# Performance work log

Measured on AMD Instinct MI355X. Metric: run time of the kernel, lower is better.

The kernel has to match this reference:

```python
import jax, jax.numpy as jnp
import numpy as np

B, L, D = 8, 2048, 1024
LN_EPS = 1e-5
WKV_EPS = 1e-8


def _ln(x, g, b):
    m = x.mean(-1, keepdims=True)
    v = x.var(-1, keepdims=True)  # biased var, matches torch LayerNorm
    return (x - m) * jax.lax.rsqrt(v + LN_EPS) * g + b


def _shift(x):
    # ZeroPad2d((0,0,1,-1)): x_prev[:, t] = x[:, t-1], x_prev[:, 0] = 0
    return jnp.pad(x, ((0, 0), (1, 0), (0, 0)))[:, :-1]


def _wkv(k, v, time_decay, time_first):
    # Faithful to the torch loop: t=0 uses exp(u + k0); t>0 decays prior state
    # (including the u-boosted first term) by exp(-exp(time_decay)).
    ew = jnp.exp(-jnp.exp(time_decay))  # [D]
    e0 = jnp.exp(time_first + k[:, 0])  # [B, D]
    a0 = e0 * v[:, 0]
    b0 = e0

    def step(carry, kv):
        a, b = carry
        kt, vt = kv
        ek = jnp.exp(kt)
        a = ew * a + ek * vt
        b = ew * b + ek
        return (a, b), a / (b + WKV_EPS)

    xs = (jnp.swapaxes(k[:, 1:], 0, 1), jnp.swapaxes(v[:, 1:], 0, 1))  # [L-1, B, D]
    _, outs = jax.lax.scan(step, (a0, b0), xs)
    out0 = (a0 / (b0 + WKV_EPS))[:, None]  # [B, 1, D]
    return jnp.concatenate([out0, jnp.swapaxes(outs, 0, 1)], axis=1)  # [B, L, D]


def setup_inputs() -> dict:
    key = jax.random.key(0)
    ks = jax.random.split(key, 10)
    s = 1.0 / np.sqrt(D)

    def w(k, shape, scale):
        return jax.random.normal(k, shape, jnp.float32) * scale

    return {
        "x": jax.random.normal(ks[0], (B, L, D), jnp.float32),
        "ln1_g": jnp.ones((D,), jnp.float32),
        "ln1_b": jnp.zeros((D,), jnp.float32),
        "Wk": w(ks[1], (D, D), s),
        "Wv": w(ks[2], (D, D), s),
        "Wr": w(ks[3], (D, D), s),
        "Wo": w(ks[4], (D, D), s),
        "time_decay": w(ks[5], (D,), 0.1),
        "time_first": w(ks[6], (D,), 0.1),
        "mix_k": jnp.full((D,), 0.5, jnp.float32),
        "mix_v": jnp.full((D,), 0.5, jnp.float32),
        "mix_r": jnp.full((D,), 0.5, jnp.float32),
        "ln2_g": jnp.ones((D,), jnp.float32),
        "ln2_b": jnp.zeros((D,), jnp.float32),
        "Wfk": w(ks[7], (D, 4 * D), s),
        "Wfv": w(ks[8], (4 * D, D), 1.0 / np.sqrt(4 * D)),
        "Wfr": w(ks[9], (D, D), s),
    }


def reference(x, ln1_g, ln1_b, Wk, Wv, Wr, Wo, time_decay, time_first,
              mix_k, mix_v, mix_r, ln2_g, ln2_b, Wfk, Wfv, Wfr):
    # --- time mixing ---
    xn = _ln(x, ln1_g, ln1_b)
    xp = _shift(xn)
    k = (xn * mix_k + xp * (1.0 - mix_k)) @ Wk
    v = (xn * mix_v + xp * (1.0 - mix_v)) @ Wv
    r = jax.nn.sigmoid((xn * mix_r + xp * (1.0 - mix_r)) @ Wr)
    wkv = _wkv(k, v, time_decay, time_first)
    x = x + (r * wkv) @ Wo
    # --- channel mixing ---
    yn = _ln(x, ln2_g, ln2_b)
    yp = _shift(yn)
    kk = jnp.square(jax.nn.relu((0.5 * yn + 0.5 * yp) @ Wfk))
    rr = jax.nn.sigmoid(yn @ Wfr)
    return x + rr * (kk @ Wfv)
```

## Files before the change

### kernel.cpp

```cpp
#include <hip/hip_runtime.h>
#include <hip/hip_bf16.h>
#include <stdint.h>

typedef __hip_bfloat16 bf16_t;
typedef __attribute__((ext_vector_type(8))) short bf16x8;
typedef __attribute__((ext_vector_type(4))) float f32x4;

#define DEV static __device__ __forceinline__

constexpr int kBB = 8, kL = 2048, kD = 1024;
constexpr int kM = kBB * kL;
constexpr int kSeg = 32, kP = 64;

DEV float bf2f(unsigned short u) { return __uint_as_float((unsigned)u << 16); }
DEV unsigned short f2bf(float f) {
  unsigned u = __float_as_uint(f);
  return (unsigned short)((u + 0x7fffu + ((u >> 16) & 1u)) >> 16);
}

DEV void gld16(const void* g, void* l) {
  const __attribute__((address_space(1))) unsigned* gp =
      (const __attribute__((address_space(1))) unsigned*)(uintptr_t)g;
  __attribute__((address_space(3))) unsigned* lp =
      (__attribute__((address_space(3))) unsigned*)(unsigned)(uintptr_t)l;
  __builtin_amdgcn_global_load_lds(gp, lp, 16, 0, 0);
}

__global__ __launch_bounds__(256) void k_transpose_cast(
    const float* __restrict__ W, bf16_t* __restrict__ Wt, int R, int C) {
  __shared__ float tile[32][33];
  const int bx = blockIdx.x * 32;
  const int by = blockIdx.y * 32;
  const int tx = threadIdx.x & 31, ty = threadIdx.x >> 5;
#pragma unroll
  for (int i = 0; i < 32; i += 8)
    tile[ty + i][tx] = W[(size_t)(by + ty + i) * C + (bx + tx)];
  __syncthreads();
#pragma unroll
  for (int i = 0; i < 32; i += 8)
    Wt[(size_t)(bx + ty + i) * R + (by + tx)] = __float2bfloat16(tile[tx][ty + i]);
}

__global__ __launch_bounds__(256) void k_ln1f(
    const float* __restrict__ X, const float* __restrict__ g, const float* __restrict__ be,
    const float* __restrict__ mk, const float* __restrict__ mv, const float* __restrict__ mr,
    bf16_t* __restrict__ ok, bf16_t* __restrict__ ov, bf16_t* __restrict__ orr) {
  const int row = blockIdx.x;
  const int l = row & (kL - 1);
  const int i = threadIdx.x;
  const bool hp = (l != 0);
  float xa[4], pa[4] = {0.f, 0.f, 0.f, 0.f};
  *(float4*)xa = ((const float4*)(X + (size_t)row * kD))[i];
  if (hp) *(float4*)pa = ((const float4*)(X + (size_t)(row - 1) * kD))[i];
  float s0 = xa[0] + xa[1] + xa[2] + xa[3];
  float q0 = xa[0] * xa[0] + xa[1] * xa[1] + xa[2] * xa[2] + xa[3] * xa[3];
  float s1 = pa[0] + pa[1] + pa[2] + pa[3];
  float q1 = pa[0] * pa[0] + pa[1] * pa[1] + pa[2] * pa[2] + pa[3] * pa[3];
#pragma unroll
  for (int off = 32; off > 0; off >>= 1) {
    s0 += __shfl_xor(s0, off); q0 += __shfl_xor(q0, off);
    s1 += __shfl_xor(s1, off); q1 += __shfl_xor(q1, off);
  }
  __shared__ float red[4][4];
  const int wid = i >> 6, lane = i & 63;
  if (lane == 0) { red[wid][0] = s0; red[wid][1] = q0; red[wid][2] = s1; red[wid][3] = q1; }
  __syncthreads();
  s0 = red[0][0] + red[1][0] + red[2][0] + red[3][0];
  q0 = red[0][1] + red[1][1] + red[2][1] + red[3][1];
  s1 = red[0][2] + red[1][2] + red[2][2] + red[3][2];
  q1 = red[0][3] + red[1][3] + red[2][3] + red[3][3];
  const float m0 = s0 * (1.f / kD);
  const float r0 = rsqrtf(fmaxf(q0 * (1.f / kD) - m0 * m0, 0.f) + 1e-5f);
  const float m1 = s1 * (1.f / kD);
  const float r1 = rsqrtf(fmaxf(q1 * (1.f / kD) - m1 * m1, 0.f) + 1e-5f);
  float ga[4], ba[4], ka[4], va[4], ra[4];
  *(float4*)ga = ((const float4*)g)[i];
  *(float4*)ba = ((const float4*)be)[i];
  *(float4*)ka = ((const float4*)mk)[i];
  *(float4*)va = ((const float4*)mv)[i];
  *(float4*)ra = ((const float4*)mr)[i];
  ushort4 uk, uv, ur;
  unsigned short* pk = (unsigned short*)&uk;
  unsigned short* pv = (unsigned short*)&uv;
  unsigned short* pr = (unsigned short*)&ur;
#pragma unroll
  for (int c = 0; c < 4; ++c) {
    float xn = (xa[c] - m0) * r0 * ga[c] + ba[c];
    float xp = hp ? (pa[c] - m1) * r1 * ga[c] + ba[c] : 0.f;
    pk[c] = f2bf(xn * ka[c] + xp * (1.f - ka[c]));
    pv[c] = f2bf(xn * va[c] + xp * (1.f - va[c]));
    pr[c] = f2bf(xn * ra[c] + xp * (1.f - ra[c]));
  }
  ((ushort4*)(ok + (size_t)row * kD))[i] = uk;
  ((ushort4*)(ov + (size_t)row * kD))[i] = uv;
  ((ushort4*)(orr + (size_t)row * kD))[i] = ur;
}

__global__ __launch_bounds__(256) void k_ln2f(
    const float* __restrict__ X, const float* __restrict__ g, const float* __restrict__ be,
    bf16_t* __restrict__ om, bf16_t* __restrict__ on) {
  const int row = blockIdx.x;
  const int l = row & (kL - 1);
  const int i = threadIdx.x;
  const bool hp = (l != 0);
  float xa[4], pa[4] = {0.f, 0.f, 0.f, 0.f};
  *(float4*)xa = ((const float4*)(X + (size_t)row * kD))[i];
  if (hp) *(float4*)pa = ((const float4*)(X + (size_t)(row - 1) * kD))[i];
  float s0 = xa[0] + xa[1] + xa[2] + xa[3];
  float q0 = xa[0] * xa[0] + xa[1] * xa[1] + xa[2] * xa[2] + xa[3] * xa[3];
  float s1 = pa[0] + pa[1] + pa[2] + pa[3];
  float q1 = pa[0] * pa[0] + pa[1] * pa[1] + pa[2] * pa[2] + pa[3] * pa[3];
#pragma unroll
  for (int off = 32; off > 0; off >>= 1) {
    s0 += __shfl_xor(s0, off); q0 += __shfl_xor(q0, off);
    s1 += __shfl_xor(s1, off); q1 += __shfl_xor(q1, off);
  }
  __shared__ float red[4][4];
  const int wid = i >> 6, lane = i & 63;
  if (lane == 0) { red[wid][0] = s0; red[wid][1] = q0; red[wid][2] = s1; red[wid][3] = q1; }
  __syncthreads();
  s0 = red[0][0] + red[1][0] + red[2][0] + red[3][0];
  q0 = red[0][1] + red[1][1] + red[2][1] + red[3][1];
  s1 = red[0][2] + red[1][2] + red[2][2] + red[3][2];
  q1 = red[0][3] + red[1][3] + red[2][3] + red[3][3];
  const float m0 = s0 * (1.f / kD);
  const float r0 = rsqrtf(fmaxf(q0 * (1.f / kD) - m0 * m0, 0.f) + 1e-5f);
  const float m1 = s1 * (1.f / kD);
  const float r1 = rsqrtf(fmaxf(q1 * (1.f / kD) - m1 * m1, 0.f) + 1e-5f);
  float ga[4], ba[4];
  *(float4*)ga = ((const float4*)g)[i];
  *(float4*)ba = ((const float4*)be)[i];
  ushort4 um, un;
  unsigned short* qm = (unsigned short*)&um;
  unsigned short* qn = (unsigned short*)&un;
#pragma unroll
  for (int c = 0; c < 4; ++c) {
    float yn = (xa[c] - m0) * r0 * ga[c] + ba[c];
    float yp = hp ? (pa[c] - m1) * r1 * ga[c] + ba[c] : 0.f;
    qm[c] = f2bf(0.5f * (yn + yp));
    qn[c] = f2bf(yn);
  }
  ((ushort4*)(om + (size_t)row * kD))[i] = um;
  ((ushort4*)(on + (size_t)row * kD))[i] = un;
}

__global__ __launch_bounds__(256) void k_wkv_seg(
    const unsigned short* __restrict__ kq, const unsigned short* __restrict__ vq,
    const float* __restrict__ td, const float* __restrict__ tf,
    float* __restrict__ segA, float* __restrict__ segB) {
  const int d = blockIdx.x * 256 + threadIdx.x;
  const int b = blockIdx.y;
  const int s = blockIdx.z;
  const float ew = __expf(-__expf(td[d]));
  const float uu = (s == 0) ? tf[d] : 0.f;
  const size_t base = ((size_t)b * kL + (size_t)s * kP) * kD + d;
  float a = 0.f, bb = 0.f;
  unsigned short kA[16], vA[16], kB[16], vB[16];
  auto pref = [&](unsigned short* ka, unsigned short* va, int c) {
    const size_t o0 = base + (size_t)c * 16 * kD;
#pragma unroll
    for (int j = 0; j < 16; ++j) {
      ka[j] = kq[o0 + (size_t)j * kD];
      va[j] = vq[o0 + (size_t)j * kD];
    }
  };
  auto comp = [&](const unsigned short* ka, const unsigned short* va, int c) {
#pragma unroll
    for (int j = 0; j < 16; ++j) {
      float kf = bf2f(ka[j]);
      if (s == 0 && c == 0 && j == 0) kf += uu;
      float ek = __expf(kf);
      a = ew * a + ek * bf2f(va[j]);
      bb = ew * bb + ek;
    }
  };
  pref(kA, vA, 0);
  pref(kB, vB, 1); comp(kA, vA, 0);
  pref(kA, vA, 2); comp(kB, vB, 1);
  pref(kB, vB, 3); comp(kA, vA, 2);
  comp(kB, vB, 3);
  const size_t sidx = ((size_t)b * kSeg + s) * kD + d;
  segA[sidx] = a;
  segB[sidx] = bb;
}

__global__ __launch_bounds__(256) void k_wkv_carry(
    const float* __restrict__ td,
    const float* __restrict__ segA, const float* __restrict__ segB,
    float* __restrict__ carA, float* __restrict__ carB) {
  const int d = blockIdx.x * 256 + threadIdx.x;
  const int b = blockIdx.y;
  const float ew = __expf(-__expf(td[d]));
  float ewP = ew;
#pragma unroll
  for (int i = 0; i < 6; ++i) ewP *= ewP;
  float ca = 0.f, cb = 0.f;
#pragma unroll 4
  for (int s = 0; s < kSeg; ++s) {
    const size_t idx = ((size_t)b * kSeg + s) * kD + d;
    carA[idx] = ca;
    carB[idx] = cb;
    ca = ewP * ca + segA[idx];
    cb = ewP * cb + segB[idx];
  }
}

__global__ __launch_bounds__(256) void k_wkv_out(
    const unsigned short* __restrict__ kq, const unsigned short* __restrict__ vq,
    const unsigned short* __restrict__ rq, const float* __restrict__ td,
    const float* __restrict__ tf, const float* __restrict__ carA,
    const float* __restrict__ carB, unsigned short* __restrict__ out) {
  const int d = blockIdx.x * 256 + threadIdx.x;
  const int b = blockIdx.y;
  const int s = blockIdx.z;
  const float ew = __expf(-__expf(td[d]));
  const float uu = (s == 0) ? tf[d] : 0.f;
  const size_t base = ((size_t)b * kL + (size_t)s * kP) * kD + d;
  const size_t sidx = ((size_t)b * kSeg + s) * kD + d;
  float a = carA[sidx], bb = carB[sidx];
  unsigned short kA[16], vA[16], rA[16], kB[16], vB[16], rB[16];
  auto pref = [&](unsigned short* ka, unsigned short* va, unsigned short* ra, int c) {
    const size_t o0 = base + (size_t)c * 16 * kD;
#pragma unroll
    for (int j = 0; j < 16; ++j) {
      ka[j] = kq[o0 + (size_t)j * kD];
      va[j] = vq[o0 + (size_t)j * kD];
      ra[j] = rq[o0 + (size_t)j * kD];
    }
  };
  auto comp = [&](const unsigned short* ka, const unsigned short* va,
                  const unsigned short* ra, int c) {
    const size_t o0 = base + (size_t)c * 16 * kD;
#pragma unroll
    for (int j = 0; j < 16; ++j) {
      float kf = bf2f(ka[j]);
      if (s == 0 && c == 0 && j == 0) kf += uu;
      float ek = __expf(kf);
      a = ew * a + ek * bf2f(va[j]);
      bb = ew * bb + ek;
      float y = a / (bb + 1e-8f);
      float sr = 1.f / (1.f + __expf(-bf2f(ra[j])));
      out[o0 + (size_t)j * kD] = f2bf(sr * y);
    }
  };
  pref(kA, vA, rA, 0);
  pref(kB, vB, rB, 1); comp(kA, vA, rA, 0);
  pref(kA, vA, rA, 2); comp(kB, vB, rB, 1);
  pref(kB, vB, rB, 3); comp(kA, vA, rA, 2);
  comp(kB, vB, rB, 3);
}

template <int EPI>
__global__ __launch_bounds__(512, 2) void gemmT(
    const bf16_t* __restrict__ A0, long strA, int lda,
    const bf16_t* __restrict__ B0, long strB, int ldb,
    bf16_t* __restrict__ Cb0, float* __restrict__ Cf, long strC,
    int N, int K, int nbx,
    const float* __restrict__ addf, const bf16_t* __restrict__ mulb) {
  __shared__ __align__(16) char lds[131072];
  const int z = blockIdx.z;
  const bf16_t* A = A0 + (size_t)z * strA;
  const bf16_t* Bt = B0 + (size_t)z * strB;
  const int nwg = gridDim.x;
  const int wg = (blockIdx.x & 7) * (nwg >> 3) + (blockIdx.x >> 3);
  const int by = wg / nbx, bx = wg - by * nbx;
  const long brow = (long)by * 256;
  const long bcol = (long)bx * 256;
  const int tid = threadIdx.x;
  const int lane = tid & 63;
  const int wid = tid >> 6;
  const int wr = wid >> 2, wc = wid & 3;

  f32x4 acc[8][4] = {};

  const int trow = tid >> 3;
  const int scol = ((tid & 7) * 16) ^ ((trow & 7) << 4);
  const char* Ag = (const char*)(A + (brow + trow) * (size_t)lda) + scol;
  const char* Bg = (const char*)(Bt + (bcol + trow) * (size_t)ldb) + scol;
  const long rsA = 64L * lda * 2;
  const long rsB = 64L * ldb * 2;

#define STAGE(kt, p)                                   \
  {                                                    \
    const long kb = (long)(kt) * 128;                  \
    char* Ld = lds + (p) * 65536 + tid * 16;           \
    gld16(Ag + kb, Ld);                                \
    gld16(Ag + kb + rsA, Ld + 8192);                   \
    gld16(Ag + kb + 2 * rsA, Ld + 16384);              \
    gld16(Ag + kb + 3 * rsA, Ld + 24576);              \
    gld16(Bg + kb, Ld + 32768);                        \
    gld16(Bg + kb + rsB, Ld + 40960);                  \
    gld16(Bg + kb + 2 * rsB, Ld + 49152);              \
    gld16(Bg + kb + 3 * rsB, Ld + 57344);              \
  }

  const int l16 = lane & 15, kq = lane >> 4;
  const int swz = (l16 & 7) << 4;
  const int oS0 = (kq * 16) ^ swz;
  const int oS1 = (64 + kq * 16) ^ swz;
  const char* Arow = lds + (wr * 128 + l16) * 128;
  const char* Brow = lds + 32768 + (wc * 64 + l16) * 128;

  bf16x8 aE[8], bE[4], aO[8], bO[4];
  const int NT = K >> 6;

  STAGE(0, 0) STAGE(1, 1)
  asm volatile("s_waitcnt vmcnt(8)" ::: "memory");
  __builtin_amdgcn_s_barrier();
#pragma unroll
  for (int m = 0; m < 8; ++m) aE[m] = *(const bf16x8*)(Arow + m * 2048 + oS0);
#pragma unroll
  for (int n = 0; n < 4; ++n) bE[n] = *(const bf16x8*)(Brow + n * 2048 + oS0);

  for (int t = 0; t < NT; ++t) {
    const int p = t & 1;
    const char* Ap = Arow + p * 65536;
    const char* Bp = Brow + p * 65536;
#pragma unroll
    for (int m = 0; m < 8; ++m) aO[m] = *(const bf16x8*)(Ap + m * 2048 + oS1);
#pragma unroll
    for (int n = 0; n < 4; ++n) bO[n] = *(const bf16x8*)(Bp + n * 2048 + oS1);
    __builtin_amdgcn_sched_barrier(0);
    __builtin_amdgcn_s_setprio(1);
#pragma unroll
    for (int m = 0; m < 8; ++m)
#pragma unroll
      for (int n = 0; n < 4; ++n)
        acc[m][n] = __builtin_amdgcn_mfma_f32_16x16x32_bf16(aE[m], bE[n], acc[m][n], 0, 0, 0);
    __builtin_amdgcn_s_setprio(0);
    asm volatile("s_waitcnt lgkmcnt(0)" ::: "memory");
    asm volatile("s_waitcnt vmcnt(0)" ::: "memory");
    __builtin_amdgcn_s_barrier();
    if (t + 2 < NT) STAGE(t + 2, p)
    if (t + 1 < NT) {
      const char* An = Arow + (1 - p) * 65536;
      const char* Bn = Brow + (1 - p) * 65536;
#pragma unroll
      for (int m = 0; m < 8; ++m) aE[m] = *(const bf16x8*)(An + m * 2048 + oS0);
#pragma unroll
      for (int n = 0; n < 4; ++n) bE[n] = *(const bf16x8*)(Bn + n * 2048 + oS0);
    }
    __builtin_amdgcn_sched_barrier(0);
    __builtin_amdgcn_s_setprio(1);
#pragma unroll
    for (int m = 0; m < 8; ++m)
#pragma unroll
      for (int n = 0; n < 4; ++n)
        acc[m][n] = __builtin_amdgcn_mfma_f32_16x16x32_bf16(aO[m], bO[n], acc[m][n], 0, 0, 0);
    __builtin_amdgcn_s_setprio(0);
  }
#undef STAGE

  bf16_t* Cb = Cb0 + (size_t)z * strC;
  const long orow = brow + wr * 128 + (lane >> 4) * 4;
  const long ocol = bcol + wc * 64 + l16;
#pragma unroll
  for (int m = 0; m < 8; ++m) {
#pragma unroll
    for (int reg = 0; reg < 4; ++reg) {
      const long r = orow + m * 16 + reg;
#pragma unroll
      for (int n = 0; n < 4; ++n) {
        const size_t idx = (size_t)r * N + ocol + n * 16;
        const float v = acc[m][n][reg];
        if constexpr (EPI == 0) {
          Cb[idx] = __float2bfloat16(v);
        } else if constexpr (EPI == 1) {
          Cf[idx] = addf[idx] + v;
        } else if constexpr (EPI == 2) {
          float u = v > 0.f ? v : 0.f;
          Cb[idx] = __float2bfloat16(u * u);
        } else if constexpr (EPI == 3) {
          Cb[idx] = __float2bfloat16(1.f / (1.f + __expf(-v)));
        } else if constexpr (EPI == 4) {
          Cf[idx] = v;
        } else {
          Cf[idx] = addf[idx] + __bfloat162float(mulb[idx]) * (Cf[idx] + v);
        }
      }
    }
  }
}

extern "C" void kernel_launch(void* const* d_in, const int* in_sizes, int n_in,
                              void* d_out, int out_size, void* d_ws, size_t ws_size,
                              hipStream_t stream) {
  const float* x    = (const float*)d_in[0];
  const float* ln1g = (const float*)d_in[1];
  const float* ln1b = (const float*)d_in[2];
  const float* Wk   = (const float*)d_in[3];
  const float* Wv   = (const float*)d_in[4];
  const float* Wr   = (const float*)d_in[5];
  const float* Wo   = (const float*)d_in[6];
  const float* td   = (const float*)d_in[7];
  const float* tf   = (const float*)d_in[8];
  const float* mk   = (const float*)d_in[9];
  const float* mv   = (const float*)d_in[10];
  const float* mr   = (const float*)d_in[11];
  const float* ln2g = (const float*)d_in[12];
  const float* ln2b = (const float*)d_in[13];
  const float* Wfk  = (const float*)d_in[14];
  const float* Wfv  = (const float*)d_in[15];
  const float* Wfr  = (const float*)d_in[16];

  char* ws = (char*)d_ws;
  const size_t MB = 1ull << 20;
  bf16_t* WkT  = (bf16_t*)(ws + 0 * MB);
  bf16_t* WvT  = (bf16_t*)(ws + 2 * MB);
  bf16_t* WrT  = (bf16_t*)(ws + 4 * MB);
  bf16_t* WoT  = (bf16_t*)(ws + 6 * MB);
  bf16_t* WfkT = (bf16_t*)(ws + 8 * MB);
  bf16_t* WfvT = (bf16_t*)(ws + 16 * MB);
  bf16_t* WfrT = (bf16_t*)(ws + 24 * MB);
  bf16_t* xk   = (bf16_t*)(ws + 28 * MB);
  bf16_t* xv   = (bf16_t*)(ws + 60 * MB);
  bf16_t* xr   = (bf16_t*)(ws + 92 * MB);
  bf16_t* kbuf = (bf16_t*)(ws + 124 * MB);
  bf16_t* vbuf = (bf16_t*)(ws + 156 * MB);
  bf16_t* rbuf = (bf16_t*)(ws + 188 * MB);
  float*  segA = (float*)(ws + 60 * MB);
  float*  segB = (float*)(ws + 61 * MB);
  float*  carA = (float*)(ws + 62 * MB);
  float*  carB = (float*)(ws + 63 * MB);
  bf16_t* rwkv = (bf16_t*)(ws + 92 * MB);
  float*  x1   = (float*)(ws + 28 * MB);
  bf16_t* rr   = (bf16_t*)(ws + 92 * MB);
  bf16_t* ynb  = (bf16_t*)(ws + 124 * MB);
  bf16_t* kk   = (bf16_t*)(ws + 124 * MB);
  bf16_t* ymix = (bf16_t*)(ws + 188 * MB);
  float*  out  = (float*)d_out;
  const long sX = (long)kM * kD;
  const long sW = (long)kD * kD;

  dim3 blk(256), blkg(512);
  k_transpose_cast<<<dim3(32, 32), blk, 0, stream>>>(Wk, WkT, 1024, 1024);
  k_transpose_cast<<<dim3(32, 32), blk, 0, stream>>>(Wv, WvT, 1024, 1024);
  k_transpose_cast<<<dim3(32, 32), blk, 0, stream>>>(Wr, WrT, 1024, 1024);
  k_transpose_cast<<<dim3(32, 32), blk, 0, stream>>>(Wo, WoT, 1024, 1024);
  k_transpose_cast<<<dim3(128, 32), blk, 0, stream>>>(Wfk, WfkT, 1024, 4096);
  k_transpose_cast<<<dim3(32, 128), blk, 0, stream>>>(Wfv, WfvT, 4096, 1024);
  k_transpose_cast<<<dim3(32, 32), blk, 0, stream>>>(Wfr, WfrT, 1024, 1024);

  k_ln1f<<<kM, blk, 0, stream>>>(x, ln1g, ln1b, mk, mv, mr, xk, xv, xr);
  gemmT<0><<<dim3(256, 1, 3), blkg, 0, stream>>>(xk, sX, 1024, WkT, sW, 1024,
      kbuf, nullptr, sX, 1024, 1024, 4, nullptr, nullptr);
  k_wkv_seg<<<dim3(4, 8, kSeg), blk, 0, stream>>>((const unsigned short*)kbuf,
      (const unsigned short*)vbuf, td, tf, segA, segB);
  k_wkv_carry<<<dim3(4, 8), blk, 0, stream>>>(td, segA, segB, carA, carB);
  k_wkv_out<<<dim3(4, 8, kSeg), blk, 0, stream>>>((const unsigned short*)kbuf,
      (const unsigned short*)vbuf, (const unsigned short*)rbuf, td, tf, carA, carB,
      (unsigned short*)rwkv);
  gemmT<1><<<256, blkg, 0, stream>>>(rwkv, 0, 1024, WoT, 0, 1024,
      nullptr, x1, 0, 1024, 1024, 4, x, nullptr);

  k_ln2f<<<kM, blk, 0, stream>>>(x1, ln2g, ln2b, ymix, ynb);
  gemmT<3><<<256, blkg, 0, stream>>>(ynb, 0, 1024, WfrT, 0, 1024,
      rr, nullptr, 0, 1024, 1024, 4, nullptr, nullptr);
  for (int c = 0; c < 2; ++c) {
    gemmT<2><<<512, blkg, 0, stream>>>(ymix, 0, 1024, WfkT + (size_t)c * 2048 * 1024, 0, 1024,
        kk, nullptr, 0, 2048, 1024, 8, nullptr, nullptr);
    if (c == 0)
      gemmT<4><<<256, blkg, 0, stream>>>(kk, 0, 2048, WfvT + 0, 0, 4096,
          nullptr, out, 0, 1024, 2048, 4, nullptr, nullptr);
    else
      gemmT<6><<<256, blkg, 0, stream>>>(kk, 0, 2048, WfvT + 2048, 0, 4096,
          nullptr, out, 0, 1024, 2048, 4, x1, rr);
  }
}
```

Baseline: 642.1 us.

## Load GEMM B operand directly from global into registers, halve LDS

The B tile is no longer staged through shared memory. Each wave loads its B fragments straight from global memory into registers every k-step, and only A is double-buffered in LDS, which halves the LDS footprint to 64KB. The aim is to cut LDS traffic and capacity so more workgroups can be resident. The cost is that B reads are no longer shared across the waves in a workgroup, so global/L2 traffic for B rises about fourfold. The uncoalesced per-lane 16-byte loads also sit on the critical path, with the vmcnt(0) wait just before the barrier.

Result: slower. 888.3 us (+38.3%).

```diff
diff --git a/kernel.cpp b/kernel.cpp
--- a/kernel.cpp
+++ b/kernel.cpp
@@ -257,7 +257,7 @@
     bf16_t* __restrict__ Cb0, float* __restrict__ Cf, long strC,
     int N, int K, int nbx,
     const float* __restrict__ addf, const bf16_t* __restrict__ mulb) {
-  __shared__ __align__(16) char lds[131072];
+  __shared__ __align__(16) char lds[65536];
   const int z = blockIdx.z;
   const bf16_t* A = A0 + (size_t)z * strA;
   const bf16_t* Bt = B0 + (size_t)z * strB;
@@ -276,50 +276,44 @@
   const int trow = tid >> 3;
   const int scol = ((tid & 7) * 16) ^ ((trow & 7) << 4);
   const char* Ag = (const char*)(A + (brow + trow) * (size_t)lda) + scol;
-  const char* Bg = (const char*)(Bt + (bcol + trow) * (size_t)ldb) + scol;
   const long rsA = 64L * lda * 2;
-  const long rsB = 64L * ldb * 2;
-
-#define STAGE(kt, p)                                   \
+
+#define STAGE_A(kt, p)                                 \
   {                                                    \
     const long kb = (long)(kt) * 128;                  \
-    char* Ld = lds + (p) * 65536 + tid * 16;           \
+    char* Ld = lds + (p) * 32768 + tid * 16;           \
     gld16(Ag + kb, Ld);                                \
     gld16(Ag + kb + rsA, Ld + 8192);                   \
     gld16(Ag + kb + 2 * rsA, Ld + 16384);              \
     gld16(Ag + kb + 3 * rsA, Ld + 24576);              \
-    gld16(Bg + kb, Ld + 32768);                        \
-    gld16(Bg + kb + rsB, Ld + 40960);                  \
-    gld16(Bg + kb + 2 * rsB, Ld + 49152);              \
-    gld16(Bg + kb + 3 * rsB, Ld + 57344);              \
   }
 
   const int l16 = lane & 15, kq = lane >> 4;
   const int swz = (l16 & 7) << 4;
   const int oS0 = (kq * 16) ^ swz;
   const int oS1 = (64 + kq * 16) ^ swz;
-  const char* Arow = lds + (wr * 128 + l16) * 128;
-  const char* Brow = lds + 32768 + (wc * 64 + l16) * 128;
-
-  bf16x8 aE[8], bE[4], aO[8], bO[4];
+  const int ArowOff = (wr * 128 + l16) * 128;
+
+  const char* Bb = (const char*)(Bt + (size_t)(bcol + wc * 64 + l16) * ldb) + kq * 16;
+  const long bstr = 16L * ldb * 2;
+
+  bf16x8 aE[8], aO[8], bE[4], bO[4];
   const int NT = K >> 6;
 
-  STAGE(0, 0) STAGE(1, 1)
-  asm volatile("s_waitcnt vmcnt(8)" ::: "memory");
+  STAGE_A(0, 0) STAGE_A(1, 1)
+#pragma unroll
+  for (int n = 0; n < 4; ++n) bE[n] = *(const bf16x8*)(Bb + n * bstr);
+  asm volatile("s_waitcnt vmcnt(0)" ::: "memory");
   __builtin_amdgcn_s_barrier();
 #pragma unroll
-  for (int m = 0; m < 8; ++m) aE[m] = *(const bf16x8*)(Arow + m * 2048 + oS0);
-#pragma unroll
-  for (int n = 0; n < 4; ++n) bE[n] = *(const bf16x8*)(Brow + n * 2048 + oS0);
+  for (int m = 0; m < 8; ++m) aE[m] = *(const bf16x8*)(lds + ArowOff + m * 2048 + oS0);
 
   for (int t = 0; t < NT; ++t) {
-    const int p = t & 1;
-    const char* Ap = Arow + p * 65536;
-    const char* Bp = Brow + p * 65536;
+    const char* Ap = lds + (t & 1) * 32768 + ArowOff;
+#pragma unroll
+    for (int n = 0; n < 4; ++n) bO[n] = *(const bf16x8*)(Bb + n * bstr + (long)t * 128 + 64);
 #pragma unroll
     for (int m = 0; m < 8; ++m) aO[m] = *(const bf16x8*)(Ap + m * 2048 + oS1);
-#pragma unroll
-    for (int n = 0; n < 4; ++n) bO[n] = *(const bf16x8*)(Bp + n * 2048 + oS1);
     __builtin_amdgcn_sched_barrier(0);
     __builtin_amdgcn_s_setprio(1);
 #pragma unroll
@@ -331,14 +325,13 @@
     asm volatile("s_waitcnt lgkmcnt(0)" ::: "memory");
     asm volatile("s_waitcnt vmcnt(0)" ::: "memory");
     __builtin_amdgcn_s_barrier();
-    if (t + 2 < NT) STAGE(t + 2, p)
+    if (t + 2 < NT) STAGE_A(t + 2, t & 1)
     if (t + 1 < NT) {
-      const char* An = Arow + (1 - p) * 65536;
-      const char* Bn = Brow + (1 - p) * 65536;
+      const char* An = lds + ((t + 1) & 1) * 32768 + ArowOff;
+#pragma unroll
+      for (int n = 0; n < 4; ++n) bE[n] = *(const bf16x8*)(Bb + n * bstr + (long)(t + 1) * 128);
 #pragma unroll
       for (int m = 0; m < 8; ++m) aE[m] = *(const bf16x8*)(An + m * 2048 + oS0);
-#pragma unroll
-      for (int n = 0; n < 4; ++n) bE[n] = *(const bf16x8*)(Bn + n * 2048 + oS0);
     }
     __builtin_amdgcn_sched_barrier(0);
     __builtin_amdgcn_s_setprio(1);
@@ -349,7 +342,7 @@
         acc[m][n] = __builtin_amdgcn_mfma_f32_16x16x32_bf16(aO[m], bO[n], acc[m][n], 0, 0, 0);
     __builtin_amdgcn_s_setprio(0);
   }
-#undef STAGE
+#undef STAGE_A
 
   bf16_t* Cb = Cb0 + (size_t)z * strC;
   const long orow = brow + wr * 128 + (lane >> 4) * 4;
```

## Switch GEMM to 32x32x16 MFMA and store residual x1 as bf16

Applied to the files above, without the earlier changes.

The GEMM inner loop moves from 16x16x32 to 32x32x16 bf16 MFMA instructions, with new LDS fragment offsets and a matching epilogue index mapping for the 16-register accumulators. Separately, the post-attention residual x1 is written as bf16 instead of fp32, and a new LayerNorm kernel and final epilogue read it as bf16. This aims at higher MFMA throughput per instruction and less memory traffic for x1. In exchange, the residual stream loses precision, which can raise output error.

New measurement: 675.5 us. +5.2%, slower.

```diff
diff --git a/kernel.cpp b/kernel.cpp
--- a/kernel.cpp
+++ b/kernel.cpp
@@ -4,7 +4,7 @@
 
 typedef __hip_bfloat16 bf16_t;
 typedef __attribute__((ext_vector_type(8))) short bf16x8;
-typedef __attribute__((ext_vector_type(4))) float f32x4;
+typedef __attribute__((ext_vector_type(16))) float f32x16;
 
 #define DEV static __device__ __forceinline__
 
@@ -96,16 +96,19 @@
   ((ushort4*)(orr + (size_t)row * kD))[i] = ur;
 }
 
-__global__ __launch_bounds__(256) void k_ln2f(
-    const float* __restrict__ X, const float* __restrict__ g, const float* __restrict__ be,
+__global__ __launch_bounds__(256) void k_ln2fb(
+    const bf16_t* __restrict__ X, const float* __restrict__ g, const float* __restrict__ be,
     bf16_t* __restrict__ om, bf16_t* __restrict__ on) {
   const int row = blockIdx.x;
   const int l = row & (kL - 1);
   const int i = threadIdx.x;
   const bool hp = (l != 0);
-  float xa[4], pa[4] = {0.f, 0.f, 0.f, 0.f};
-  *(float4*)xa = ((const float4*)(X + (size_t)row * kD))[i];
-  if (hp) *(float4*)pa = ((const float4*)(X + (size_t)(row - 1) * kD))[i];
+  ushort4 xu = ((const ushort4*)(X + (size_t)row * kD))[i];
+  ushort4 pu = make_ushort4(0, 0, 0, 0);
+  if (hp) pu = ((const ushort4*)(X + (size_t)(row - 1) * kD))[i];
+  float xa[4], pa[4];
+  xa[0] = bf2f(xu.x); xa[1] = bf2f(xu.y); xa[2] = bf2f(xu.z); xa[3] = bf2f(xu.w);
+  pa[0] = bf2f(pu.x); pa[1] = bf2f(pu.y); pa[2] = bf2f(pu.z); pa[3] = bf2f(pu.w);
   float s0 = xa[0] + xa[1] + xa[2] + xa[3];
   float q0 = xa[0] * xa[0] + xa[1] * xa[1] + xa[2] * xa[2] + xa[3] * xa[3];
   float s1 = pa[0] + pa[1] + pa[2] + pa[3];
@@ -256,7 +259,8 @@
     const bf16_t* __restrict__ B0, long strB, int ldb,
     bf16_t* __restrict__ Cb0, float* __restrict__ Cf, long strC,
     int N, int K, int nbx,
-    const float* __restrict__ addf, const bf16_t* __restrict__ mulb) {
+    const float* __restrict__ addf, const bf16_t* __restrict__ addb,
+    const bf16_t* __restrict__ mulb) {
   __shared__ __align__(16) char lds[131072];
   const int z = blockIdx.z;
   const bf16_t* A = A0 + (size_t)z * strA;
@@ -271,7 +275,7 @@
   const int wid = tid >> 6;
   const int wr = wid >> 2, wc = wid & 3;
 
-  f32x4 acc[8][4] = {};
+  f32x16 acc[4][2] = {};
 
   const int trow = tid >> 3;
   const int scol = ((tid & 7) * 16) ^ ((trow & 7) << 4);
@@ -294,12 +298,15 @@
     gld16(Bg + kb + 3 * rsB, Ld + 57344);              \
   }
 
-  const int l16 = lane & 15, kq = lane >> 4;
-  const int swz = (l16 & 7) << 4;
-  const int oS0 = (kq * 16) ^ swz;
-  const int oS1 = (64 + kq * 16) ^ swz;
-  const char* Arow = lds + (wr * 128 + l16) * 128;
-  const char* Brow = lds + 32768 + (wc * 64 + l16) * 128;
+  const int l31 = lane & 31;
+  const int kh = lane >> 5;
+  const int swz = (lane & 7) << 4;
+  const int o0 = (0 * 32 + kh * 16) ^ swz;
+  const int o1 = (1 * 32 + kh * 16) ^ swz;
+  const int o2 = (2 * 32 + kh * 16) ^ swz;
+  const int o3 = (3 * 32 + kh * 16) ^ swz;
+  const char* Arow = lds + (wr * 128 + l31) * 128;
+  const char* Brow = lds + 32768 + (wc * 64 + l31) * 128;
 
   bf16x8 aE[8], bE[4], aO[8], bO[4];
   const int NT = K >> 6;
@@ -308,25 +315,39 @@
   asm volatile("s_waitcnt vmcnt(8)" ::: "memory");
   __builtin_amdgcn_s_barrier();
 #pragma unroll
-  for (int m = 0; m < 8; ++m) aE[m] = *(const bf16x8*)(Arow + m * 2048 + oS0);
-#pragma unroll
-  for (int n = 0; n < 4; ++n) bE[n] = *(const bf16x8*)(Brow + n * 2048 + oS0);
+  for (int mt = 0; mt < 4; ++mt) {
+    aE[mt * 2] = *(const bf16x8*)(Arow + mt * 4096 + o0);
+    aE[mt * 2 + 1] = *(const bf16x8*)(Arow + mt * 4096 + o1);
+  }
+#pragma unroll
+  for (int nt = 0; nt < 2; ++nt) {
+    bE[nt * 2] = *(const bf16x8*)(Brow + nt * 4096 + o0);
+    bE[nt * 2 + 1] = *(const bf16x8*)(Brow + nt * 4096 + o1);
+  }
 
   for (int t = 0; t < NT; ++t) {
     const int p = t & 1;
     const char* Ap = Arow + p * 65536;
     const char* Bp = Brow + p * 65536;
 #pragma unroll
-    for (int m = 0; m < 8; ++m) aO[m] = *(const bf16x8*)(Ap + m * 2048 + oS1);
-#pragma unroll
-    for (int n = 0; n < 4; ++n) bO[n] = *(const bf16x8*)(Bp + n * 2048 + oS1);
+    for (int mt = 0; mt < 4; ++mt) {
+      aO[mt * 2] = *(const bf16x8*)(Ap + mt * 4096 + o2);
+      aO[mt * 2 + 1] = *(const bf16x8*)(Ap + mt * 4096 + o3);
+    }
+#pragma unroll
+    for (int nt = 0; nt < 2; ++nt) {
+      bO[nt * 2] = *(const bf16x8*)(Bp + nt * 4096 + o2);
+      bO[nt * 2 + 1] = *(const bf16x8*)(Bp + nt * 4096 + o3);
+    }
     __builtin_amdgcn_sched_barrier(0);
     __builtin_amdgcn_s_setprio(1);
 #pragma unroll
-    for (int m = 0; m < 8; ++m)
-#pragma unroll
-      for (int n = 0; n < 4; ++n)
-        acc[m][n] = __builtin_amdgcn_mfma_f32_16x16x32_bf16(aE[m], bE[n], acc[m][n], 0, 0, 0);
+    for (int mt = 0; mt < 4; ++mt)
+#pragma unroll
+      for (int nt = 0; nt < 2; ++nt) {
+        acc[mt][nt] = __builtin_amdgcn_mfma_f32_32x32x16_bf16(aE[mt * 2], bE[nt * 2], acc[mt][nt], 0, 0, 0);
+        acc[mt][nt] = __builtin_amdgcn_mfma_f32_32x32x16_bf16(aE[mt * 2 + 1], bE[nt * 2 + 1], acc[mt][nt], 0, 0, 0);
+      }
     __builtin_amdgcn_s_setprio(0);
     asm volatile("s_waitcnt lgkmcnt(0)" ::: "memory");
     asm volatile("s_waitcnt vmcnt(0)" ::: "memory");
@@ -336,37 +357,45 @@
       const char* An = Arow + (1 - p) * 65536;
       const char* Bn = Brow + (1 - p) * 65536;
 #pragma unroll
-      for (int m = 0; m < 8; ++m) aE[m] = *(const bf16x8*)(An + m * 2048 + oS0);
-#pragma unroll
-      for (int n = 0; n < 4; ++n) bE[n] = *(const bf16x8*)(Bn + n * 2048 + oS0);
+      for (int mt = 0; mt < 4; ++mt) {
+        aE[mt * 2] = *(const bf16x8*)(An + mt * 4096 + o0);
+        aE[mt * 2 + 1] = *(const bf16x8*)(An + mt * 4096 + o1);
+      }
+#pragma unroll
+      for (int nt = 0; nt < 2; ++nt) {
+        bE[nt * 2] = *(const bf16x8*)(Bn + nt * 4096 + o0);
+        bE[nt * 2 + 1] = *(const bf16x8*)(Bn + nt * 4096 + o1);
+      }
     }
     __builtin_amdgcn_sched_barrier(0);
     __builtin_amdgcn_s_setprio(1);
 #pragma unroll
-    for (int m = 0; m < 8; ++m)
-#pragma unroll
-      for (int n = 0; n < 4; ++n)
-        acc[m][n] = __builtin_amdgcn_mfma_f32_16x16x32_bf16(aO[m], bO[n], acc[m][n], 0, 0, 0);
+    for (int mt = 0; mt < 4; ++mt)
+#pragma unroll
+      for (int nt = 0; nt < 2; ++nt) {
+        acc[mt][nt] = __builtin_amdgcn_mfma_f32_32x32x16_bf16(aO[mt * 2], bO[nt * 2], acc[mt][nt], 0, 0, 0);
+        acc[mt][nt] = __builtin_amdgcn_mfma_f32_32x32x16_bf16(aO[mt * 2 + 1], bO[nt * 2 + 1], acc[mt][nt], 0, 0, 0);
+      }
     __builtin_amdgcn_s_setprio(0);
   }
 #undef STAGE
 
   bf16_t* Cb = Cb0 + (size_t)z * strC;
-  const long orow = brow + wr * 128 + (lane >> 4) * 4;
-  const long ocol = bcol + wc * 64 + l16;
-#pragma unroll
-  for (int m = 0; m < 8; ++m) {
-#pragma unroll
-    for (int reg = 0; reg < 4; ++reg) {
-      const long r = orow + m * 16 + reg;
-#pragma unroll
-      for (int n = 0; n < 4; ++n) {
-        const size_t idx = (size_t)r * N + ocol + n * 16;
-        const float v = acc[m][n][reg];
+  const long orow = brow + wr * 128 + 4 * kh;
+  const long ocol = bcol + wc * 64 + l31;
+#pragma unroll
+  for (int mt = 0; mt < 4; ++mt) {
+#pragma unroll
+    for (int reg = 0; reg < 16; ++reg) {
+      const long r = orow + mt * 32 + (reg & 3) + 8 * (reg >> 2);
+#pragma unroll
+      for (int nt = 0; nt < 2; ++nt) {
+        const size_t idx = (size_t)r * N + ocol + nt * 32;
+        const float v = acc[mt][nt][reg];
         if constexpr (EPI == 0) {
           Cb[idx] = __float2bfloat16(v);
         } else if constexpr (EPI == 1) {
-          Cf[idx] = addf[idx] + v;
+          Cb[idx] = __float2bfloat16(addf[idx] + v);
         } else if constexpr (EPI == 2) {
           float u = v > 0.f ? v : 0.f;
           Cb[idx] = __float2bfloat16(u * u);
@@ -375,7 +404,7 @@
         } else if constexpr (EPI == 4) {
           Cf[idx] = v;
         } else {
-          Cf[idx] = addf[idx] + __bfloat162float(mulb[idx]) * (Cf[idx] + v);
+          Cf[idx] = __bfloat162float(addb[idx]) + __bfloat162float(mulb[idx]) * (Cf[idx] + v);
         }
       }
     }
@@ -423,7 +452,7 @@
   float*  carA = (float*)(ws + 62 * MB);
   float*  carB = (float*)(ws + 63 * MB);
   bf16_t* rwkv = (bf16_t*)(ws + 92 * MB);
-  float*  x1   = (float*)(ws + 28 * MB);
+  bf16_t* x1b  = (bf16_t*)(ws + 28 * MB);
   bf16_t* rr   = (bf16_t*)(ws + 92 * MB);
   bf16_t* ynb  = (bf16_t*)(ws + 124 * MB);
   bf16_t* kk   = (bf16_t*)(ws + 124 * MB);
@@ -443,7 +472,7 @@
 
   k_ln1f<<<kM, blk, 0, stream>>>(x, ln1g, ln1b, mk, mv, mr, xk, xv, xr);
   gemmT<0><<<dim3(256, 1, 3), blkg, 0, stream>>>(xk, sX, 1024, WkT, sW, 1024,
-      kbuf, nullptr, sX, 1024, 1024, 4, nullptr, nullptr);
+      kbuf, nullptr, sX, 1024, 1024, 4, nullptr, nullptr, nullptr);
   k_wkv_seg<<<dim3(4, 8, kSeg), blk, 0, stream>>>((const unsigned short*)kbuf,
       (const unsigned short*)vbuf, td, tf, segA, segB);
   k_wkv_carry<<<dim3(4, 8), blk, 0, stream>>>(td, segA, segB, carA, carB);
@@ -451,19 +480,19 @@
       (const unsigned short*)vbuf, (const unsigned short*)rbuf, td, tf, carA, carB,
       (unsigned short*)rwkv);
   gemmT<1><<<256, blkg, 0, stream>>>(rwkv, 0, 1024, WoT, 0, 1024,
-      nullptr, x1, 0, 1024, 1024, 4, x, nullptr);
-
-  k_ln2f<<<kM, blk, 0, stream>>>(x1, ln2g, ln2b, ymix, ynb);
+      x1b, nullptr, 0, 1024, 1024, 4, x, nullptr, nullptr);
+
+  k_ln2fb<<<kM, blk, 0, stream>>>(x1b, ln2g, ln2b, ymix, ynb);
   gemmT<3><<<256, blkg, 0, stream>>>(ynb, 0, 1024, WfrT, 0, 1024,
-      rr, nullptr, 0, 1024, 1024, 4, nullptr, nullptr);
+      rr, nullptr, 0, 1024, 1024, 4, nullptr, nullptr, nullptr);
   for (int c = 0; c < 2; ++c) {
     gemmT<2><<<512, blkg, 0, stream>>>(ymix, 0, 1024, WfkT + (size_t)c * 2048 * 1024, 0, 1024,
-        kk, nullptr, 0, 2048, 1024, 8, nullptr, nullptr);
+        kk, nullptr, 0, 2048, 1024, 8, nullptr, nullptr, nullptr);
     if (c == 0)
       gemmT<4><<<256, blkg, 0, stream>>>(kk, 0, 2048, WfvT + 0, 0, 4096,
-          nullptr, out, 0, 1024, 2048, 4, nullptr, nullptr);
+          nullptr, out, 0, 1024, 2048, 4, nullptr, nullptr, nullptr);
     else
       gemmT<6><<<256, blkg, 0, stream>>>(kk, 0, 2048, WfvT + 2048, 0, 4096,
-          nullptr, out, 0, 1024, 2048, 4, x1, rr);
-  }
-}
+          nullptr, out, 0, 1024, 2048, 4, nullptr, x1b, rr);
+  }
+}
```
